# Performance work log

Hardware: AMD Instinct MI355X
Metric: run time of the kernel (lower is better)

Reference implementation:

```python
import jax, jax.numpy as jnp
import numpy as np
import math

D_MODEL = 2048
NUM_HEADS = 16
D_FF = 8192
HEAD_DIM = D_MODEL // NUM_HEADS
EPS = 1e-5


def _xavier(key, out_f, in_f):
    std = math.sqrt(2.0 / (in_f + out_f))
    return jax.random.normal(key, (out_f, in_f), dtype=jnp.float32) * std


def setup_inputs() -> dict:
    key = jax.random.key(0)
    ks = jax.random.split(key, 8)
    x = jax.random.normal(ks[0], (2, 2048, D_MODEL), dtype=jnp.float32)
    return {
        "x": x,
        "Wq": _xavier(ks[1], D_MODEL, D_MODEL),
        "Wk": _xavier(ks[2], D_MODEL, D_MODEL),
        "Wv": _xavier(ks[3], D_MODEL, D_MODEL),
        "Wo": _xavier(ks[4], D_MODEL, D_MODEL),
        "W1": _xavier(ks[5], D_FF, D_MODEL),
        "W2": _xavier(ks[6], D_MODEL, D_FF),
        "g1": jnp.ones((D_MODEL,), jnp.float32),
        "b1": jnp.zeros((D_MODEL,), jnp.float32),
        "g2": jnp.ones((D_MODEL,), jnp.float32),
        "b2": jnp.zeros((D_MODEL,), jnp.float32),
    }


def _ternary(w):
    # per-tensor abs-mean threshold -> {-1, 0, 1}
    abs_w = jnp.abs(w)
    thr = jnp.mean(abs_w)
    return jnp.where(abs_w > thr, jnp.sign(w), jnp.zeros_like(w))


def _tlin(x, w):
    # F.linear with ternarized weight [out, in], no bias
    return jnp.einsum("bsi,oi->bso", x, _ternary(w))


def _layernorm(x, g, b):
    mu = jnp.mean(x, axis=-1, keepdims=True)
    var = jnp.mean(jnp.square(x - mu), axis=-1, keepdims=True)
    return (x - mu) * jax.lax.rsqrt(var + EPS) * g + b


def reference(x, Wq, Wk, Wv, Wo, W1, W2, g1, b1, g2, b2):
    B, S, D = x.shape
    H, Hd = NUM_HEADS, HEAD_DIM
    q = _tlin(x, Wq).reshape(B, S, H, Hd).transpose(0, 2, 1, 3)  # bhsd
    k = _tlin(x, Wk).reshape(B, S, H, Hd).transpose(0, 2, 1, 3)
    v = _tlin(x, Wv).reshape(B, S, H, Hd).transpose(0, 2, 1, 3)
    scores = jnp.einsum("bhqd,bhkd->bhqk", q, k) / math.sqrt(Hd)
    probs = jax.nn.softmax(scores, axis=-1)
    attn = jnp.einsum("bhqk,bhkd->bhqd", probs, v)
    attn = attn.transpose(0, 2, 1, 3).reshape(B, S, D)
    attn = _tlin(attn, Wo)
    x = _layernorm(x + attn, g1, b1)  # dropout is identity in eval
    ff = _tlin(jax.nn.relu(_tlin(x, W1)), W2)
    x = _layernorm(x + ff, g2, b2)
    return x
```

## Files before the change

kernel.cpp:

```cpp
#include <hip/hip_runtime.h>
#include <hip/hip_bf16.h>

typedef __bf16 bf16_t;
typedef __bf16 bf16x8 __attribute__((ext_vector_type(8)));
typedef __bf16 bf16x4 __attribute__((ext_vector_type(4)));
typedef float f32x4 __attribute__((ext_vector_type(4)));
typedef int i32x4 __attribute__((ext_vector_type(4)));

__device__ __forceinline__ f32x4 mfma16(bf16x8 a, bf16x8 b, f32x4 c) {
  return __builtin_amdgcn_mfma_f32_16x16x32_bf16(a, b, c, 0, 0, 0);
}

__device__ __forceinline__ void gload16(const void* g, void* l) {
  __builtin_amdgcn_global_load_lds(
      (const __attribute__((address_space(1))) void*)g,
      (__attribute__((address_space(3))) void*)l, 16, 0, 0);
}

__global__ void abssum_all(const float* __restrict__ W0, const float* __restrict__ W1_,
                           const float* __restrict__ W2_, const float* __restrict__ W3,
                           const float* __restrict__ W4, const float* __restrict__ W5,
                           double* __restrict__ partial) {
  __shared__ double sd[256];
  const int w = blockIdx.y, tid = threadIdx.x;
  const float* W = (w == 0) ? W0 : (w == 1) ? W1_ : (w == 2) ? W2_ : (w == 3) ? W3 : (w == 4) ? W4 : W5;
  const int n4 = (w < 4) ? 1048576 : 4194304;
  double s = 0.0;
  for (int i = blockIdx.x * 256 + tid; i < n4; i += 262144) {
    float4 v = ((const float4*)W)[i];
    s += (double)fabsf(v.x); s += (double)fabsf(v.y);
    s += (double)fabsf(v.z); s += (double)fabsf(v.w);
  }
  sd[tid] = s; __syncthreads();
  for (int st = 128; st > 0; st >>= 1) { if (tid < st) sd[tid] += sd[tid + st]; __syncthreads(); }
  if (tid == 0) partial[w * 1024 + blockIdx.x] = sd[0];
}

__global__ void abssum_fin(const double* __restrict__ partial, double* __restrict__ sums) {
  __shared__ double sd[256];
  const int tid = threadIdx.x;
  const double* p = partial + blockIdx.x * 1024;
  double s = p[tid] + p[tid + 256] + p[tid + 512] + p[tid + 768];
  sd[tid] = s; __syncthreads();
  for (int st = 128; st > 0; st >>= 1) { if (tid < st) sd[tid] += sd[tid + st]; __syncthreads(); }
  if (tid == 0) sums[blockIdx.x] = sd[0];
}

__global__ void ternarize4(const float* __restrict__ W0, const float* __restrict__ W1_,
                           const float* __restrict__ W2_, const float* __restrict__ W3,
                           bf16_t* __restrict__ out, const double* __restrict__ sums) {
  const int w = blockIdx.x >> 12;
  const float* W = (w == 0) ? W0 : (w == 1) ? W1_ : (w == 2) ? W2_ : W3;
  const double thr = sums[w] / 4194304.0;
  const int i = (blockIdx.x & 4095) * 256 + threadIdx.x;
  float4 v = ((const float4*)W)[i];
  bf16x4 o;
  float t;
  t = ((double)fabsf(v.x) > thr) ? (v.x > 0.f ? 1.f : -1.f) : 0.f; o[0] = (bf16_t)t;
  t = ((double)fabsf(v.y) > thr) ? (v.y > 0.f ? 1.f : -1.f) : 0.f; o[1] = (bf16_t)t;
  t = ((double)fabsf(v.z) > thr) ? (v.z > 0.f ? 1.f : -1.f) : 0.f; o[2] = (bf16_t)t;
  t = ((double)fabsf(v.w) > thr) ? (v.w > 0.f ? 1.f : -1.f) : 0.f; o[3] = (bf16_t)t;
  *(bf16x4*)&out[(size_t)w * 4194304 + (size_t)i * 4] = o;
}

__global__ void ternarize_k(const float* __restrict__ W, bf16_t* __restrict__ out,
                            const double* __restrict__ sum, double n) {
  const double thr = sum[0] / n;
  const int i = blockIdx.x * 256 + threadIdx.x;
  float4 v = ((const float4*)W)[i];
  bf16x4 o;
  float t;
  t = ((double)fabsf(v.x) > thr) ? (v.x > 0.f ? 1.f : -1.f) : 0.f; o[0] = (bf16_t)t;
  t = ((double)fabsf(v.y) > thr) ? (v.y > 0.f ? 1.f : -1.f) : 0.f; o[1] = (bf16_t)t;
  t = ((double)fabsf(v.z) > thr) ? (v.z > 0.f ? 1.f : -1.f) : 0.f; o[2] = (bf16_t)t;
  t = ((double)fabsf(v.w) > thr) ? (v.w > 0.f ? 1.f : -1.f) : 0.f; o[3] = (bf16_t)t;
  *(bf16x4*)&out[(size_t)i * 4] = o;
}

__global__ void split_x_k(const float* __restrict__ X, bf16_t* __restrict__ xhl) {
  const int i = blockIdx.x * 256 + threadIdx.x;
  const int t = i >> 9, col = (i & 511) * 4;
  float4 v = ((const float4*)X)[i];
  bf16x4 h, l;
  h[0] = (bf16_t)v.x; l[0] = (bf16_t)(v.x - (float)h[0]);
  h[1] = (bf16_t)v.y; l[1] = (bf16_t)(v.y - (float)h[1]);
  h[2] = (bf16_t)v.z; l[2] = (bf16_t)(v.z - (float)h[2]);
  h[3] = (bf16_t)v.w; l[3] = (bf16_t)(v.w - (float)h[3]);
  *(bf16x4*)&xhl[(size_t)t * 4096 + col] = h;
  *(bf16x4*)&xhl[(size_t)t * 4096 + 2048 + col] = l;
}

template <int EPI>
__global__ __launch_bounds__(512, 2) void gemmP(
    const bf16_t* __restrict__ Ah, const bf16_t* __restrict__ Bw,
    void* __restrict__ C0, int N, int K, int lda) {
  constexpr int BM = 128;
  __shared__ __align__(16) bf16_t sA[3][BM * 64];
  __shared__ __align__(16) bf16_t sB[3][256 * 64];

  const int tid = threadIdx.x;
  const int wid = tid >> 6, lane = tid & 63, lr = lane & 15, lg = lane >> 4;
  const int wr = wid >> 2, wc = wid & 3;
  const size_t Ks = (size_t)K;

  const int nwg = gridDim.x * gridDim.y;
  const int bid0 = blockIdx.y * gridDim.x + blockIdx.x;
  const int swz = (bid0 & 7) * (nwg >> 3) + (bid0 >> 3);
  const int bx = swz % gridDim.x, by = swz / gridDim.x;
  const size_t m0 = (size_t)by * BM, n0 = (size_t)bx * 256;
  const int nt = K / 64;

  f32x4 acc[4][4] = {};

  auto STAGEH = [&](int bi, int kt, int half) {
    const size_t ko = (size_t)kt * 64;
    if (half == 0) {
#pragma unroll
      for (int i = 0; i < 2; i++) {
        const int t = i * 512 + tid;
        const int r = t >> 3;
        const int su = (t & 7) ^ (r & 7);
        const int lo = (i * 512 + wid * 64) * 8;
        gload16(Ah + (m0 + r) * (size_t)lda + ko + su * 8, (void*)&sA[bi][lo]);
      }
      {
        const int r = tid >> 3;
        const int su = (tid & 7) ^ (r & 7);
        gload16(Bw + (n0 + r) * Ks + ko + su * 8, (void*)&sB[bi][(wid * 64) * 8]);
      }
    } else {
#pragma unroll
      for (int i = 1; i < 4; i++) {
        const int t = i * 512 + tid;
        const int r = t >> 3;
        const int su = (t & 7) ^ (r & 7);
        gload16(Bw + (n0 + r) * Ks + ko + su * 8, (void*)&sB[bi][(i * 512 + wid * 64) * 8]);
      }
    }
  };
  auto LDA = [&](const bf16_t* base, int m, int k) -> bf16x8 {
    const int row = wr * 64 + m * 16 + lr;
    const int u = (k * 4 + lg) ^ (lr & 7);
    return *(const bf16x8*)&base[row * 64 + u * 8];
  };
  auto LDB = [&](const bf16_t* base, int n, int k) -> bf16x8 {
    const int row = wc * 64 + n * 16 + lr;
    const int u = (k * 4 + lg) ^ (lr & 7);
    return *(const bf16x8*)&base[row * 64 + u * 8];
  };

  STAGEH(0, 0, 0); STAGEH(0, 0, 1);
  STAGEH(1, 1, 0); STAGEH(1, 1, 1);
  asm volatile("s_waitcnt vmcnt(6)" ::: "memory");
  __builtin_amdgcn_s_barrier();

  int bc = 0, bs = 2;
  for (int kt = 0; kt < nt; kt++) {
    const bool pf = (kt + 2 < nt);
    bf16x8 a[4][2], bfr[4][2];
#pragma unroll
    for (int m = 0; m < 4; m++)
#pragma unroll
      for (int k = 0; k < 2; k++) a[m][k] = LDA(&sA[bc][0], m, k);
#pragma unroll
    for (int n = 0; n < 2; n++)
#pragma unroll
      for (int k = 0; k < 2; k++) bfr[n][k] = LDB(&sB[bc][0], n, k);
    if (pf) STAGEH(bs, kt + 2, 0);
    __builtin_amdgcn_s_barrier();
    asm volatile("s_waitcnt lgkmcnt(0)" ::: "memory");
    __builtin_amdgcn_sched_barrier(0);
    __builtin_amdgcn_s_setprio(1);
#pragma unroll
    for (int k = 0; k < 2; k++)
#pragma unroll
      for (int m = 0; m < 4; m++)
#pragma unroll
        for (int n = 0; n < 2; n++) acc[m][n] = mfma16(a[m][k], bfr[n][k], acc[m][n]);
    __builtin_amdgcn_s_setprio(0);
    __builtin_amdgcn_s_barrier();
#pragma unroll
    for (int n = 0; n < 2; n++)
#pragma unroll
      for (int k = 0; k < 2; k++) bfr[n + 2][k] = LDB(&sB[bc][0], n + 2, k);
    if (pf) STAGEH(bs, kt + 2, 1);
    if (kt + 1 < nt) {
      if (pf) asm volatile("s_waitcnt vmcnt(6)" ::: "memory");
      else    asm volatile("s_waitcnt vmcnt(0)" ::: "memory");
    }
    __builtin_amdgcn_s_barrier();
    asm volatile("s_waitcnt lgkmcnt(0)" ::: "memory");
    __builtin_amdgcn_sched_barrier(0);
    __builtin_amdgcn_s_setprio(1);
#pragma unroll
    for (int k = 0; k < 2; k++)
#pragma unroll
      for (int m = 0; m < 4; m++)
#pragma unroll
        for (int n = 0; n < 2; n++) acc[m][n + 2] = mfma16(a[m][k], bfr[n + 2][k], acc[m][n + 2]);
    __builtin_amdgcn_s_setprio(0);
    __builtin_amdgcn_s_barrier();
    bc = (bc + 1 == 3) ? 0 : bc + 1;
    bs = (bs + 1 == 3) ? 0 : bs + 1;
  }

  const int row0 = (int)m0 + wr * 64, colb = (int)n0 + wc * 64;
#pragma unroll
  for (int m = 0; m < 4; m++)
#pragma unroll
    for (int n = 0; n < 4; n++)
#pragma unroll
      for (int j = 0; j < 4; j++) {
        const int r = row0 + m * 16 + lg * 4 + j;
        const int c = colb + n * 16 + lr;
        const float v = acc[m][n][j];
        if constexpr (EPI == 1) {
          const int bb = r >> 11, ss = r & 2047;
          ((bf16_t*)C0)[((size_t)bb * 2048 + c) * 2048 + ss] = (bf16_t)v;
        } else {
          ((float*)C0)[(size_t)r * N + c] = v;
        }
      }
}

template <int EPI, int MB>
__global__ __launch_bounds__(512, 2) void gemm256(
    const bf16_t* __restrict__ A, const bf16_t* __restrict__ Bw,
    void* __restrict__ C0, void* __restrict__ C1,
    int N, int K, int lda, int ldb) {
  __shared__ __align__(16) bf16_t sA[2][256 * 64];
  __shared__ __align__(16) bf16_t sB[2][256 * 64];
  const int tid = threadIdx.x;
  const int wid = tid >> 6, lane = tid & 63, lr = lane & 15, lg = lane >> 4;
  const int wr = wid >> 2, wc = wid & 3;
  const int nwg = gridDim.x * gridDim.y;
  const int bid0 = blockIdx.y * gridDim.x + blockIdx.x;
  const int swz = (bid0 & 7) * (nwg >> 3) + (bid0 >> 3);
  const int bx = swz % gridDim.x, by = swz / gridDim.x;
  const int mt = by & ((1 << MB) - 1), kh = by >> MB;
  const int koff = kh * K;
  const size_t m0 = (size_t)mt * 256, n0 = (size_t)bx * 256;
  const int nt = K / 64;
  const bf16_t* Abase = A + m0 * (size_t)lda;
  const bf16_t* Bbase = Bw + n0 * (size_t)ldb;

  f32x4 acc[8][4] = {};

  auto SG = [&](const bf16_t* base, bf16_t* dst, int kt, int h, int ld) {
    const size_t co = (size_t)((kt * 64 + koff) & (ld - 1));
#pragma unroll
    for (int i = 0; i < 2; i++) {
      const int e = (2 * h + i) * 512 + tid;
      const int r = e >> 3;
      const int su = (tid & 7) ^ (r & 7);
      gload16(base + (size_t)r * ld + co + su * 8,
              (void*)&dst[((2 * h + i) * 512 + wid * 64) * 8]);
    }
  };
  auto LDA = [&](int bi, int m, int k) -> bf16x8 {
    const int row = wr * 128 + m * 16 + lr;
    const int u = (k * 4 + lg) ^ (lr & 7);
    return *(const bf16x8*)&sA[bi][row * 64 + u * 8];
  };
  auto LDB = [&](int bi, int n, int k) -> bf16x8 {
    const int row = wc * 64 + n * 16 + lr;
    const int u = (k * 4 + lg) ^ (lr & 7);
    return *(const bf16x8*)&sB[bi][row * 64 + u * 8];
  };

  SG(Abase, sA[0], 0, 0, lda); SG(Abase, sA[0], 0, 1, lda);
  SG(Bbase, sB[0], 0, 0, ldb); SG(Bbase, sB[0], 0, 1, ldb);
  SG(Bbase, sB[1], 1, 0, ldb); SG(Bbase, sB[1], 1, 1, ldb); SG(Abase, sA[1], 1, 0, lda);
  asm volatile("s_waitcnt vmcnt(6)" ::: "memory");
  __builtin_amdgcn_s_barrier();

  for (int kt = 0; kt < nt; kt++) {
    const int bi = kt & 1, bn = bi ^ 1;
    bf16x8 a[4][2], b[4][2];
#pragma unroll
    for (int m = 0; m < 4; m++)
#pragma unroll
      for (int k = 0; k < 2; k++) a[m][k] = LDA(bi, m, k);
#pragma unroll
    for (int n = 0; n < 2; n++)
#pragma unroll
      for (int k = 0; k < 2; k++) b[n][k] = LDB(bi, n, k);
    if (kt + 1 < nt) SG(Abase, sA[bn], kt + 1, 1, lda);
    __builtin_amdgcn_s_barrier();
    asm volatile("s_waitcnt lgkmcnt(0)" ::: "memory");
    __builtin_amdgcn_sched_barrier(0);
    __builtin_amdgcn_s_setprio(1);
#pragma unroll
    for (int k = 0; k < 2; k++)
#pragma unroll
      for (int m = 0; m < 4; m++)
#pragma unroll
        for (int n = 0; n < 2; n++) acc[m][n] = mfma16(a[m][k], b[n][k], acc[m][n]);
    __builtin_amdgcn_s_setprio(0);
    __builtin_amdgcn_s_barrier();
#pragma unroll
    for (int n = 0; n < 2; n++)
#pragma unroll
      for (int k = 0; k < 2; k++) b[n + 2][k] = LDB(bi, n + 2, k);
    if (kt + 2 < nt) SG(Bbase, sB[bi], kt + 2, 0, ldb);
    __builtin_amdgcn_s_barrier();
    asm volatile("s_waitcnt lgkmcnt(0)" ::: "memory");
    __builtin_amdgcn_sched_barrier(0);
    __builtin_amdgcn_s_setprio(1);
#pragma unroll
    for (int k = 0; k < 2; k++)
#pragma unroll
      for (int m = 0; m < 4; m++)
#pragma unroll
        for (int n = 0; n < 2; n++) acc[m][n + 2] = mfma16(a[m][k], b[n + 2][k], acc[m][n + 2]);
    __builtin_amdgcn_s_setprio(0);
    __builtin_amdgcn_s_barrier();
#pragma unroll
    for (int m = 0; m < 4; m++)
#pragma unroll
      for (int k = 0; k < 2; k++) a[m][k] = LDA(bi, m + 4, k);
    if (kt + 2 < nt) SG(Bbase, sB[bi], kt + 2, 1, ldb);
    __builtin_amdgcn_s_barrier();
    asm volatile("s_waitcnt lgkmcnt(0)" ::: "memory");
    __builtin_amdgcn_sched_barrier(0);
    __builtin_amdgcn_s_setprio(1);
#pragma unroll
    for (int k = 0; k < 2; k++)
#pragma unroll
      for (int m = 0; m < 4; m++)
#pragma unroll
        for (int n = 0; n < 2; n++) acc[m + 4][n + 2] = mfma16(a[m][k], b[n + 2][k], acc[m + 4][n + 2]);
    __builtin_amdgcn_s_setprio(0);
    __builtin_amdgcn_s_barrier();
    if (kt + 2 < nt) SG(Abase, sA[bi], kt + 2, 0, lda);
    __builtin_amdgcn_s_setprio(1);
#pragma unroll
    for (int k = 0; k < 2; k++)
#pragma unroll
      for (int m = 0; m < 4; m++)
#pragma unroll
        for (int n = 0; n < 2; n++) acc[m + 4][n] = mfma16(a[m][k], b[n][k], acc[m + 4][n]);
    __builtin_amdgcn_s_setprio(0);
    if (kt + 1 < nt) {
      if (kt + 2 < nt) asm volatile("s_waitcnt vmcnt(6)" ::: "memory");
      else             asm volatile("s_waitcnt vmcnt(0)" ::: "memory");
    }
    __builtin_amdgcn_s_barrier();
  }

  const int row0 = (int)m0 + wr * 128, colb = (int)n0 + wc * 64;
#pragma unroll
  for (int m = 0; m < 8; m++)
#pragma unroll
    for (int n = 0; n < 4; n++)
#pragma unroll
      for (int j = 0; j < 4; j++) {
        const int r = row0 + m * 16 + lg * 4 + j;
        const int c = colb + n * 16 + lr;
        const float v = acc[m][n][j];
        if constexpr (EPI == 0) {
          bf16_t hi = (bf16_t)v;
          ((bf16_t*)C0)[(size_t)r * N + c] = hi;
          ((bf16_t*)C1)[(size_t)r * N + c] = (bf16_t)(v - (float)hi);
        } else if constexpr (EPI == 4) {
          float* dst = (float*)(kh ? C1 : C0);
          dst[(size_t)r * N + c] = v;
        } else {
          ((bf16_t*)C0)[(size_t)r * N + c] = (bf16_t)fmaxf(v, 0.f);
        }
      }
}

__global__ __launch_bounds__(256, 2) void attn_k(
    const bf16_t* __restrict__ qh, const bf16_t* __restrict__ ql,
    const bf16_t* __restrict__ kh, const bf16_t* __restrict__ kl,
    const bf16_t* __restrict__ vT, bf16_t* __restrict__ out) {
  __shared__ __align__(16) bf16_t sKh[2 * 8192];
  __shared__ __align__(16) bf16_t sKl[2 * 8192];
  __shared__ __align__(16) bf16_t plds[4][2048];

  const int fid = blockIdx.y * 16 + blockIdx.x;
  const int qt = fid >> 5;
  const int bh = (fid & 7) * 4 + ((fid >> 3) & 3);
  const int b = bh >> 4, h = bh & 15;
  const int wv = threadIdx.x >> 6, lane = threadIdx.x & 63, lr = lane & 15, lg = lane >> 4;
  const size_t tok0 = (size_t)b * 2048 + qt * 128 + wv * 16;
  bf16_t* pw = &plds[wv][0];

  auto STAGE = [&](int bufi, int kv0n) {
#pragma unroll
    for (int i = 0; i < 4; i++) {
      const int tt = wv * 4 + i;
      const int r = tt * 4 + (lane >> 4);
      const int ce = ((lane & 15) ^ (r & 7)) * 8;
      const size_t gofs = ((size_t)b * 2048 + kv0n + r) * 4096 + h * 128 + ce;
      gload16(kh + gofs, (void*)&sKh[bufi * 8192 + tt * 512]);
      gload16(kl + gofs, (void*)&sKl[bufi * 8192 + tt * 512]);
    }
  };

  bf16x8 qhf[2][4], qlf[2][4];
#pragma unroll
  for (int t = 0; t < 2; t++) {
    const bf16_t* qp = qh + (tok0 + t * 64 + lr) * 4096 + h * 128 + lg * 8;
    const bf16_t* qp2 = ql + (tok0 + t * 64 + lr) * 4096 + h * 128 + lg * 8;
#pragma unroll
    for (int ks = 0; ks < 4; ks++) {
      qhf[t][ks] = *(const bf16x8*)(qp + ks * 32);
      qlf[t][ks] = *(const bf16x8*)(qp2 + ks * 32);
    }
  }
  f32x4 oacc[2][8] = {};
  float mrun[2] = {-1e30f, -1e30f};
  float lrun[2] = {0.f, 0.f};
  const bf16_t* vbase = vT + ((size_t)b * 2048 + h * 128) * 2048;
  const float sc = 0.08838834764831845f;
  const int swz8 = 2 * (lr & 7);

  STAGE(0, 0);
  for (int c = 0; c < 32; c++) {
    const int kv0 = c * 64;
    if (c + 1 < 32) {
      STAGE((c + 1) & 1, kv0 + 64);
      asm volatile("s_waitcnt vmcnt(8)" ::: "memory");
    } else {
      asm volatile("s_waitcnt vmcnt(0)" ::: "memory");
    }
    __builtin_amdgcn_s_barrier();

    const int bufo = (c & 1) * 8192;
    f32x4 s[2][4] = {};
    __builtin_amdgcn_s_setprio(1);
#pragma unroll
    for (int nb = 0; nb < 4; nb++) {
      const int rbase = bufo + (nb * 16 + lr) * 128;
#pragma unroll
      for (int ks = 0; ks < 4; ks++) {
        const int u = (((ks * 4 + lg) ^ (lr & 7)) * 8);
        bf16x8 kf = *(const bf16x8*)&sKh[rbase + u];
        bf16x8 kg = *(const bf16x8*)&sKl[rbase + u];
        s[0][nb] = mfma16(kf, qhf[0][ks], s[0][nb]);
        s[1][nb] = mfma16(kf, qhf[1][ks], s[1][nb]);
        s[0][nb] = mfma16(kf, qlf[0][ks], s[0][nb]);
        s[1][nb] = mfma16(kf, qlf[1][ks], s[1][nb]);
        s[0][nb] = mfma16(kg, qhf[0][ks], s[0][nb]);
        s[1][nb] = mfma16(kg, qhf[1][ks], s[1][nb]);
      }
    }
    __builtin_amdgcn_s_setprio(0);

    float resc[2];
    bool skip[2];
#pragma unroll
    for (int t = 0; t < 2; t++) {
#pragma unroll
      for (int nb = 0; nb < 4; nb++) s[t][nb] *= sc;
      f32x4 m4 = __builtin_elementwise_max(
          __builtin_elementwise_max(s[t][0], s[t][1]),
          __builtin_elementwise_max(s[t][2], s[t][3]));
      float mx = fmaxf(fmaxf(m4[0], m4[1]), fmaxf(m4[2], m4[3]));
      mx = fmaxf(mx, __shfl_xor(mx, 16));
      mx = fmaxf(mx, __shfl_xor(mx, 32));
      skip[t] = (__all(mx <= mrun[t] + 8.f) != 0);
      float rs_ = 1.f;
      if (!skip[t]) {
        const float mnew = fmaxf(mrun[t], mx);
        rs_ = __expf(mrun[t] - mnew);
        mrun[t] = mnew;
      }
      resc[t] = rs_;
      float ls = 0.f;
#pragma unroll
      for (int nb = 0; nb < 4; nb++) {
        bf16x4 pk;
#pragma unroll
        for (int j = 0; j < 4; j++) {
          const float p = __expf(s[t][nb][j] - mrun[t]);
          ls += p;
          pk[j] = (bf16_t)p;
        }
        const int s8 = (4 * nb + lg) ^ swz8;
        *(bf16x4*)&pw[t * 1024 + lr * 64 + s8 * 4] = pk;
      }
      ls += __shfl_xor(ls, 16);
      ls += __shfl_xor(ls, 32);
      lrun[t] = lrun[t] * rs_ + ls;
    }
    asm volatile("s_waitcnt lgkmcnt(0)" ::: "memory");
    __builtin_amdgcn_sched_barrier(0);
    bf16x8 pfr[2][2];
#pragma unroll
    for (int t = 0; t < 2; t++)
#pragma unroll
      for (int kc = 0; kc < 2; kc++) {
        const int se = (8 * kc + 2 * lg) ^ swz8;
        pfr[t][kc] = *(const bf16x8*)&pw[t * 1024 + lr * 64 + se * 4];
      }
    if (!skip[0]) {
#pragma unroll
      for (int dt = 0; dt < 8; dt++) oacc[0][dt] *= resc[0];
    }
    if (!skip[1]) {
#pragma unroll
      for (int dt = 0; dt < 8; dt++) oacc[1][dt] *= resc[1];
    }

    const bf16_t* vp = vbase + kv0 + lg * 8;
    __builtin_amdgcn_s_setprio(1);
#pragma unroll
    for (int dt = 0; dt < 8; dt++) {
      const bf16_t* vr = vp + (size_t)(dt * 16 + lr) * 2048;
      bf16x8 v0 = *(const bf16x8*)(vr);
      bf16x8 v1 = *(const bf16x8*)(vr + 32);
      oacc[0][dt] = mfma16(v0, pfr[0][0], oacc[0][dt]);
      oacc[1][dt] = mfma16(v0, pfr[1][0], oacc[1][dt]);
      oacc[0][dt] = mfma16(v1, pfr[0][1], oacc[0][dt]);
      oacc[1][dt] = mfma16(v1, pfr[1][1], oacc[1][dt]);
    }
    __builtin_amdgcn_s_setprio(0);
    asm volatile("" ::: "memory");
    __builtin_amdgcn_s_barrier();
  }

  {
    bf16_t* ep = &sKh[wv * 2176];
    const int q = lane >> 2, c4 = lane & 3;
    const int qs = 2 * (q & 7);
#pragma unroll
    for (int t = 0; t < 2; t++) {
      const float inv = 1.f / lrun[t];
#pragma unroll
      for (int dt = 0; dt < 8; dt++) {
        bf16x4 pk;
#pragma unroll
        for (int j = 0; j < 4; j++) pk[j] = (bf16_t)(oacc[t][dt][j] * inv);
        const int s5 = (4 * dt + lg) ^ swz8;
        *(bf16x4*)&ep[lr * 136 + s5 * 4] = pk;
      }
      asm volatile("s_waitcnt lgkmcnt(0)" ::: "memory");
      __builtin_amdgcn_sched_barrier(0);
      bf16_t* orow = out + (tok0 + t * 64 + q) * 2048 + h * 128 + c4 * 32;
#pragma unroll
      for (int i = 0; i < 4; i++) {
        const int se = (c4 * 8 + 2 * i) ^ qs;
        bf16x8 vv = *(const bf16x8*)&ep[q * 136 + se * 4];
        *(bf16x8*)(orow + i * 8) = vv;
      }
      asm volatile("s_waitcnt lgkmcnt(0)" ::: "memory");
    }
  }
}

__global__ __launch_bounds__(256) void ln_k(
    const float* __restrict__ X, const float* __restrict__ R,
    const float* __restrict__ G, const float* __restrict__ Bt,
    float* __restrict__ O32, bf16_t* __restrict__ O16) {
  const int t = blockIdx.x, tid = threadIdx.x;
  const float4* xp = (const float4*)(X + (size_t)t * 2048);
  const float4* rp = (const float4*)(R + (size_t)t * 2048);
  float4 v0 = xp[tid], w0 = rp[tid];
  float4 v1 = xp[tid + 256], w1 = rp[tid + 256];
  v0.x += w0.x; v0.y += w0.y; v0.z += w0.z; v0.w += w0.w;
  v1.x += w1.x; v1.y += w1.y; v1.z += w1.z; v1.w += w1.w;
  float sum = v0.x + v0.y + v0.z + v0.w + v1.x + v1.y + v1.z + v1.w;
  float sq = v0.x * v0.x + v0.y * v0.y + v0.z * v0.z + v0.w * v0.w +
             v1.x * v1.x + v1.y * v1.y + v1.z * v1.z + v1.w * v1.w;
  for (int d = 1; d < 64; d <<= 1) { sum += __shfl_xor(sum, d); sq += __shfl_xor(sq, d); }
  __shared__ float s1[4], s2[4];
  const int wv = tid >> 6, lane = tid & 63;
  if (lane == 0) { s1[wv] = sum; s2[wv] = sq; }
  __syncthreads();
  const float tot = s1[0] + s1[1] + s1[2] + s1[3];
  const float tsq = s2[0] + s2[1] + s2[2] + s2[3];
  const float mu = tot * (1.f / 2048.f);
  const float var = tsq * (1.f / 2048.f) - mu * mu;
  const float rs = 1.f / sqrtf(var + 1e-5f);
  const float4* gp = (const float4*)G;
  const float4* bp = (const float4*)Bt;
  float4 g0 = gp[tid], g1v = gp[tid + 256], b0 = bp[tid], b1v = bp[tid + 256];
  float4 o0, o1;
  o0.x = (v0.x - mu) * rs * g0.x + b0.x; o0.y = (v0.y - mu) * rs * g0.y + b0.y;
  o0.z = (v0.z - mu) * rs * g0.z + b0.z; o0.w = (v0.w - mu) * rs * g0.w + b0.w;
  o1.x = (v1.x - mu) * rs * g1v.x + b1v.x; o1.y = (v1.y - mu) * rs * g1v.y + b1v.y;
  o1.z = (v1.z - mu) * rs * g1v.z + b1v.z; o1.w = (v1.w - mu) * rs * g1v.w + b1v.w;
  if (O32) {
    ((float4*)(O32 + (size_t)t * 2048))[tid] = o0;
    ((float4*)(O32 + (size_t)t * 2048))[tid + 256] = o1;
  }
  if (O16) {
    bf16x4 h0, h1;
    h0[0] = (bf16_t)o0.x; h0[1] = (bf16_t)o0.y; h0[2] = (bf16_t)o0.z; h0[3] = (bf16_t)o0.w;
    h1[0] = (bf16_t)o1.x; h1[1] = (bf16_t)o1.y; h1[2] = (bf16_t)o1.z; h1[3] = (bf16_t)o1.w;
    *(bf16x4*)&O16[(size_t)t * 2048 + tid * 4] = h0;
    *(bf16x4*)&O16[(size_t)t * 2048 + 1024 + tid * 4] = h1;
  }
}

__global__ __launch_bounds__(256) void ln2_k(
    const bf16_t* __restrict__ Xb, const float* __restrict__ R0, const float* __restrict__ R1,
    const float* __restrict__ G, const float* __restrict__ Bt, float* __restrict__ out) {
  const int t = blockIdx.x, tid = threadIdx.x;
  bf16x4 x0 = *(const bf16x4*)&Xb[(size_t)t * 2048 + tid * 4];
  bf16x4 x1 = *(const bf16x4*)&Xb[(size_t)t * 2048 + 1024 + tid * 4];
  const float4* r0p = (const float4*)(R0 + (size_t)t * 2048);
  const float4* r1p = (const float4*)(R1 + (size_t)t * 2048);
  float4 a0 = r0p[tid], a1 = r0p[tid + 256];
  float4 c0 = r1p[tid], c1 = r1p[tid + 256];
  float4 v0, v1;
  v0.x = (float)x0[0] + a0.x + c0.x; v0.y = (float)x0[1] + a0.y + c0.y;
  v0.z = (float)x0[2] + a0.z + c0.z; v0.w = (float)x0[3] + a0.w + c0.w;
  v1.x = (float)x1[0] + a1.x + c1.x; v1.y = (float)x1[1] + a1.y + c1.y;
  v1.z = (float)x1[2] + a1.z + c1.z; v1.w = (float)x1[3] + a1.w + c1.w;
  float sum = v0.x + v0.y + v0.z + v0.w + v1.x + v1.y + v1.z + v1.w;
  float sq = v0.x * v0.x + v0.y * v0.y + v0.z * v0.z + v0.w * v0.w +
             v1.x * v1.x + v1.y * v1.y + v1.z * v1.z + v1.w * v1.w;
  for (int d = 1; d < 64; d <<= 1) { sum += __shfl_xor(sum, d); sq += __shfl_xor(sq, d); }
  __shared__ float s1[4], s2[4];
  const int wv = tid >> 6, lane = tid & 63;
  if (lane == 0) { s1[wv] = sum; s2[wv] = sq; }
  __syncthreads();
  const float tot = s1[0] + s1[1] + s1[2] + s1[3];
  const float tsq = s2[0] + s2[1] + s2[2] + s2[3];
  const float mu = tot * (1.f / 2048.f);
  const float var = tsq * (1.f / 2048.f) - mu * mu;
  const float rs = 1.f / sqrtf(var + 1e-5f);
  const float4* gp = (const float4*)G;
  const float4* bp = (const float4*)Bt;
  float4 g0 = gp[tid], g1v = gp[tid + 256], b0 = bp[tid], b1v = bp[tid + 256];
  float4 o0, o1;
  o0.x = (v0.x - mu) * rs * g0.x + b0.x; o0.y = (v0.y - mu) * rs * g0.y + b0.y;
  o0.z = (v0.z - mu) * rs * g0.z + b0.z; o0.w = (v0.w - mu) * rs * g0.w + b0.w;
  o1.x = (v1.x - mu) * rs * g1v.x + b1v.x; o1.y = (v1.y - mu) * rs * g1v.y + b1v.y;
  o1.z = (v1.z - mu) * rs * g1v.z + b1v.z; o1.w = (v1.w - mu) * rs * g1v.w + b1v.w;
  ((float4*)(out + (size_t)t * 2048))[tid] = o0;
  ((float4*)(out + (size_t)t * 2048))[tid + 256] = o1;
}

extern "C" void kernel_launch(void* const* d_in, const int* in_sizes, int n_in,
                              void* d_out, int out_size, void* d_ws, size_t ws_size,
                              hipStream_t stream) {
  const float* x  = (const float*)d_in[0];
  const float* Wq = (const float*)d_in[1];
  const float* Wk = (const float*)d_in[2];
  const float* Wv = (const float*)d_in[3];
  const float* Wo = (const float*)d_in[4];
  const float* W1 = (const float*)d_in[5];
  const float* W2 = (const float*)d_in[6];
  const float* g1 = (const float*)d_in[7];
  const float* b1 = (const float*)d_in[8];
  const float* g2 = (const float*)d_in[9];
  const float* b2 = (const float*)d_in[10];
  float* out = (float*)d_out;
  char* ws = (char*)d_ws;

  constexpr size_t SZB = (size_t)4096 * 2048 * 2;
  bf16_t* xhl = (bf16_t*)(ws + 0 * SZB);
  bf16_t* qkh = (bf16_t*)(ws + 2 * SZB);
  bf16_t* qkl = (bf16_t*)(ws + 4 * SZB);
  bf16_t* vt  = (bf16_t*)(ws + 6 * SZB);
  bf16_t* at  = (bf16_t*)(ws + 7 * SZB);
  float* o32  = (float*)(ws + 8 * SZB);
  bf16_t* wt  = (bf16_t*)(ws + 8 * SZB + (size_t)4096 * 2048 * 4);
  double* red = (double*)(ws + 8 * SZB + (size_t)4096 * 2048 * 4 + (size_t)8192 * 2048 * 2);
  double* sums = red + 8192;
  bf16_t* h1b = qkh;
  bf16_t* f1 = (bf16_t*)(ws + 4 * SZB);
  float* g32a = o32;
  float* g32b = (float*)(ws + 0 * SZB);
  (void)in_sizes; (void)n_in; (void)out_size; (void)ws_size;

  abssum_all<<<dim3(1024, 6), 256, 0, stream>>>(Wq, Wk, Wv, Wo, W1, W2, red);
  abssum_fin<<<6, 256, 0, stream>>>(red, sums);
  split_x_k<<<8192, 256, 0, stream>>>(x, xhl);
  ternarize4<<<16384, 256, 0, stream>>>(Wq, Wk, Wv, Wo, wt, sums);

  gemm256<0, 8><<<dim3(16, 16), 512, 0, stream>>>(xhl, wt, qkh, qkl, 4096, 4096, 4096, 2048);
  gemmP<1><<<dim3(8, 32), 512, 0, stream>>>(xhl, wt + 8388608, vt, 2048, 2048, 4096);
  attn_k<<<dim3(16, 32), 256, 0, stream>>>(qkh, qkl, qkh + 2048, qkl + 2048, vt, at);
  gemmP<2><<<dim3(8, 32), 512, 0, stream>>>(at, wt + 12582912, o32, 2048, 2048, 2048);
  ln_k<<<4096, 256, 0, stream>>>(x, o32, g1, b1, nullptr, h1b);
  ternarize_k<<<16384, 256, 0, stream>>>(W1, wt, sums + 4, 16777216.0);
  gemm256<3, 8><<<dim3(32, 16), 512, 0, stream>>>(h1b, wt, f1, nullptr, 8192, 2048, 2048, 2048);
  ternarize_k<<<16384, 256, 0, stream>>>(W2, wt, sums + 5, 16777216.0);
  gemm256<4, 4><<<dim3(8, 32), 512, 0, stream>>>(f1, wt, g32a, g32b, 2048, 4096, 8192, 8192);
  ln2_k<<<4096, 256, 0, stream>>>(h1b, g32a, g32b, g2, b2, out);
}
```

Measured before the change: 780.3 us.

## Fuse QKV projections into one GEMM and split-K the output projection

The Q/K and V projections now run as one wide GEMM launch. Its epilogue writes hi/lo bf16 split outputs for Q and K and a transposed bf16 V. The Wo projection moves from the 128-row gemmP kernel to the split-K gemm256 kernel, writing two fp32 partials that the new ln1 kernel sums along with the residual. This cuts launches, fills the GPU better with larger tiles, and removes the gemmP kernel. The cost is an extra fp32 partial buffer read in layernorm and a branchy epilogue.

After: 887.6 us. 1.14x slower.

```diff
diff --git a/kernel.cpp b/kernel.cpp
--- a/kernel.cpp
+++ b/kernel.cpp
@@ -90,143 +90,10 @@
   *(bf16x4*)&xhl[(size_t)t * 4096 + 2048 + col] = l;
 }
 
-template <int EPI>
-__global__ __launch_bounds__(512, 2) void gemmP(
-    const bf16_t* __restrict__ Ah, const bf16_t* __restrict__ Bw,
-    void* __restrict__ C0, int N, int K, int lda) {
-  constexpr int BM = 128;
-  __shared__ __align__(16) bf16_t sA[3][BM * 64];
-  __shared__ __align__(16) bf16_t sB[3][256 * 64];
-
-  const int tid = threadIdx.x;
-  const int wid = tid >> 6, lane = tid & 63, lr = lane & 15, lg = lane >> 4;
-  const int wr = wid >> 2, wc = wid & 3;
-  const size_t Ks = (size_t)K;
-
-  const int nwg = gridDim.x * gridDim.y;
-  const int bid0 = blockIdx.y * gridDim.x + blockIdx.x;
-  const int swz = (bid0 & 7) * (nwg >> 3) + (bid0 >> 3);
-  const int bx = swz % gridDim.x, by = swz / gridDim.x;
-  const size_t m0 = (size_t)by * BM, n0 = (size_t)bx * 256;
-  const int nt = K / 64;
-
-  f32x4 acc[4][4] = {};
-
-  auto STAGEH = [&](int bi, int kt, int half) {
-    const size_t ko = (size_t)kt * 64;
-    if (half == 0) {
-#pragma unroll
-      for (int i = 0; i < 2; i++) {
-        const int t = i * 512 + tid;
-        const int r = t >> 3;
-        const int su = (t & 7) ^ (r & 7);
-        const int lo = (i * 512 + wid * 64) * 8;
-        gload16(Ah + (m0 + r) * (size_t)lda + ko + su * 8, (void*)&sA[bi][lo]);
-      }
-      {
-        const int r = tid >> 3;
-        const int su = (tid & 7) ^ (r & 7);
-        gload16(Bw + (n0 + r) * Ks + ko + su * 8, (void*)&sB[bi][(wid * 64) * 8]);
-      }
-    } else {
-#pragma unroll
-      for (int i = 1; i < 4; i++) {
-        const int t = i * 512 + tid;
-        const int r = t >> 3;
-        const int su = (t & 7) ^ (r & 7);
-        gload16(Bw + (n0 + r) * Ks + ko + su * 8, (void*)&sB[bi][(i * 512 + wid * 64) * 8]);
-      }
-    }
-  };
-  auto LDA = [&](const bf16_t* base, int m, int k) -> bf16x8 {
-    const int row = wr * 64 + m * 16 + lr;
-    const int u = (k * 4 + lg) ^ (lr & 7);
-    return *(const bf16x8*)&base[row * 64 + u * 8];
-  };
-  auto LDB = [&](const bf16_t* base, int n, int k) -> bf16x8 {
-    const int row = wc * 64 + n * 16 + lr;
-    const int u = (k * 4 + lg) ^ (lr & 7);
-    return *(const bf16x8*)&base[row * 64 + u * 8];
-  };
-
-  STAGEH(0, 0, 0); STAGEH(0, 0, 1);
-  STAGEH(1, 1, 0); STAGEH(1, 1, 1);
-  asm volatile("s_waitcnt vmcnt(6)" ::: "memory");
-  __builtin_amdgcn_s_barrier();
-
-  int bc = 0, bs = 2;
-  for (int kt = 0; kt < nt; kt++) {
-    const bool pf = (kt + 2 < nt);
-    bf16x8 a[4][2], bfr[4][2];
-#pragma unroll
-    for (int m = 0; m < 4; m++)
-#pragma unroll
-      for (int k = 0; k < 2; k++) a[m][k] = LDA(&sA[bc][0], m, k);
-#pragma unroll
-    for (int n = 0; n < 2; n++)
-#pragma unroll
-      for (int k = 0; k < 2; k++) bfr[n][k] = LDB(&sB[bc][0], n, k);
-    if (pf) STAGEH(bs, kt + 2, 0);
-    __builtin_amdgcn_s_barrier();
-    asm volatile("s_waitcnt lgkmcnt(0)" ::: "memory");
-    __builtin_amdgcn_sched_barrier(0);
-    __builtin_amdgcn_s_setprio(1);
-#pragma unroll
-    for (int k = 0; k < 2; k++)
-#pragma unroll
-      for (int m = 0; m < 4; m++)
-#pragma unroll
-        for (int n = 0; n < 2; n++) acc[m][n] = mfma16(a[m][k], bfr[n][k], acc[m][n]);
-    __builtin_amdgcn_s_setprio(0);
-    __builtin_amdgcn_s_barrier();
-#pragma unroll
-    for (int n = 0; n < 2; n++)
-#pragma unroll
-      for (int k = 0; k < 2; k++) bfr[n + 2][k] = LDB(&sB[bc][0], n + 2, k);
-    if (pf) STAGEH(bs, kt + 2, 1);
-    if (kt + 1 < nt) {
-      if (pf) asm volatile("s_waitcnt vmcnt(6)" ::: "memory");
-      else    asm volatile("s_waitcnt vmcnt(0)" ::: "memory");
-    }
-    __builtin_amdgcn_s_barrier();
-    asm volatile("s_waitcnt lgkmcnt(0)" ::: "memory");
-    __builtin_amdgcn_sched_barrier(0);
-    __builtin_amdgcn_s_setprio(1);
-#pragma unroll
-    for (int k = 0; k < 2; k++)
-#pragma unroll
-      for (int m = 0; m < 4; m++)
-#pragma unroll
-        for (int n = 0; n < 2; n++) acc[m][n + 2] = mfma16(a[m][k], bfr[n + 2][k], acc[m][n + 2]);
-    __builtin_amdgcn_s_setprio(0);
-    __builtin_amdgcn_s_barrier();
-    bc = (bc + 1 == 3) ? 0 : bc + 1;
-    bs = (bs + 1 == 3) ? 0 : bs + 1;
-  }
-
-  const int row0 = (int)m0 + wr * 64, colb = (int)n0 + wc * 64;
-#pragma unroll
-  for (int m = 0; m < 4; m++)
-#pragma unroll
-    for (int n = 0; n < 4; n++)
-#pragma unroll
-      for (int j = 0; j < 4; j++) {
-        const int r = row0 + m * 16 + lg * 4 + j;
-        const int c = colb + n * 16 + lr;
-        const float v = acc[m][n][j];
-        if constexpr (EPI == 1) {
-          const int bb = r >> 11, ss = r & 2047;
-          ((bf16_t*)C0)[((size_t)bb * 2048 + c) * 2048 + ss] = (bf16_t)v;
-        } else {
-          ((float*)C0)[(size_t)r * N + c] = v;
-        }
-      }
-}
-
 template <int EPI, int MB>
 __global__ __launch_bounds__(512, 2) void gemm256(
     const bf16_t* __restrict__ A, const bf16_t* __restrict__ Bw,
-    void* __restrict__ C0, void* __restrict__ C1,
+    void* __restrict__ C0, void* __restrict__ C1, void* __restrict__ C2,
     int N, int K, int lda, int ldb) {
   __shared__ __align__(16) bf16_t sA[2][256 * 64];
   __shared__ __align__(16) bf16_t sB[2][256 * 64];
@@ -358,10 +225,15 @@
         const int r = row0 + m * 16 + lg * 4 + j;
         const int c = colb + n * 16 + lr;
         const float v = acc[m][n][j];
-        if constexpr (EPI == 0) {
-          bf16_t hi = (bf16_t)v;
-          ((bf16_t*)C0)[(size_t)r * N + c] = hi;
-          ((bf16_t*)C1)[(size_t)r * N + c] = (bf16_t)(v - (float)hi);
+        if constexpr (EPI == 5) {
+          if (c < 4096) {
+            bf16_t hi = (bf16_t)v;
+            ((bf16_t*)C0)[(size_t)r * 4096 + c] = hi;
+            ((bf16_t*)C1)[(size_t)r * 4096 + c] = (bf16_t)(v - (float)hi);
+          } else {
+            const int bb = r >> 11, ss = r & 2047;
+            ((bf16_t*)C2)[((size_t)bb * 2048 + (c - 4096)) * 2048 + ss] = (bf16_t)v;
+          }
         } else if constexpr (EPI == 4) {
           float* dst = (float*)(kh ? C1 : C0);
           dst[(size_t)r * N + c] = v;
@@ -551,17 +423,18 @@
   }
 }
 
-__global__ __launch_bounds__(256) void ln_k(
-    const float* __restrict__ X, const float* __restrict__ R,
-    const float* __restrict__ G, const float* __restrict__ Bt,
-    float* __restrict__ O32, bf16_t* __restrict__ O16) {
+__global__ __launch_bounds__(256) void ln1_k(
+    const float* __restrict__ X, const float* __restrict__ R0, const float* __restrict__ R1,
+    const float* __restrict__ G, const float* __restrict__ Bt, bf16_t* __restrict__ O16) {
   const int t = blockIdx.x, tid = threadIdx.x;
   const float4* xp = (const float4*)(X + (size_t)t * 2048);
-  const float4* rp = (const float4*)(R + (size_t)t * 2048);
-  float4 v0 = xp[tid], w0 = rp[tid];
-  float4 v1 = xp[tid + 256], w1 = rp[tid + 256];
-  v0.x += w0.x; v0.y += w0.y; v0.z += w0.z; v0.w += w0.w;
-  v1.x += w1.x; v1.y += w1.y; v1.z += w1.z; v1.w += w1.w;
+  const float4* r0p = (const float4*)(R0 + (size_t)t * 2048);
+  const float4* r1p = (const float4*)(R1 + (size_t)t * 2048);
+  float4 v0 = xp[tid], v1 = xp[tid + 256];
+  float4 a0 = r0p[tid], a1 = r0p[tid + 256];
+  float4 c0 = r1p[tid], c1 = r1p[tid + 256];
+  v0.x += a0.x + c0.x; v0.y += a0.y + c0.y; v0.z += a0.z + c0.z; v0.w += a0.w + c0.w;
+  v1.x += a1.x + c1.x; v1.y += a1.y + c1.y; v1.z += a1.z + c1.z; v1.w += a1.w + c1.w;
   float sum = v0.x + v0.y + v0.z + v0.w + v1.x + v1.y + v1.z + v1.w;
   float sq = v0.x * v0.x + v0.y * v0.y + v0.z * v0.z + v0.w * v0.w +
              v1.x * v1.x + v1.y * v1.y + v1.z * v1.z + v1.w * v1.w;
@@ -578,22 +451,17 @@
   const float4* gp = (const float4*)G;
   const float4* bp = (const float4*)Bt;
   float4 g0 = gp[tid], g1v = gp[tid + 256], b0 = bp[tid], b1v = bp[tid + 256];
-  float4 o0, o1;
-  o0.x = (v0.x - mu) * rs * g0.x + b0.x; o0.y = (v0.y - mu) * rs * g0.y + b0.y;
-  o0.z = (v0.z - mu) * rs * g0.z + b0.z; o0.w = (v0.w - mu) * rs * g0.w + b0.w;
-  o1.x = (v1.x - mu) * rs * g1v.x + b1v.x; o1.y = (v1.y - mu) * rs * g1v.y + b1v.y;
-  o1.z = (v1.z - mu) * rs * g1v.z + b1v.z; o1.w = (v1.w - mu) * rs * g1v.w + b1v.w;
-  if (O32) {
-    ((float4*)(O32 + (size_t)t * 2048))[tid] = o0;
-    ((float4*)(O32 + (size_t)t * 2048))[tid + 256] = o1;
-  }
-  if (O16) {
-    bf16x4 h0, h1;
-    h0[0] = (bf16_t)o0.x; h0[1] = (bf16_t)o0.y; h0[2] = (bf16_t)o0.z; h0[3] = (bf16_t)o0.w;
-    h1[0] = (bf16_t)o1.x; h1[1] = (bf16_t)o1.y; h1[2] = (bf16_t)o1.z; h1[3] = (bf16_t)o1.w;
-    *(bf16x4*)&O16[(size_t)t * 2048 + tid * 4] = h0;
-    *(bf16x4*)&O16[(size_t)t * 2048 + 1024 + tid * 4] = h1;
-  }
+  bf16x4 h0, h1;
+  h0[0] = (bf16_t)((v0.x - mu) * rs * g0.x + b0.x);
+  h0[1] = (bf16_t)((v0.y - mu) * rs * g0.y + b0.y);
+  h0[2] = (bf16_t)((v0.z - mu) * rs * g0.z + b0.z);
+  h0[3] = (bf16_t)((v0.w - mu) * rs * g0.w + b0.w);
+  h1[0] = (bf16_t)((v1.x - mu) * rs * g1v.x + b1v.x);
+  h1[1] = (bf16_t)((v1.y - mu) * rs * g1v.y + b1v.y);
+  h1[2] = (bf16_t)((v1.z - mu) * rs * g1v.z + b1v.z);
+  h1[3] = (bf16_t)((v1.w - mu) * rs * g1v.w + b1v.w);
+  *(bf16x4*)&O16[(size_t)t * 2048 + tid * 4] = h0;
+  *(bf16x4*)&O16[(size_t)t * 2048 + 1024 + tid * 4] = h1;
 }
 
 __global__ __launch_bounds__(256) void ln2_k(
@@ -665,8 +533,8 @@
   double* sums = red + 8192;
   bf16_t* h1b = qkh;
   bf16_t* f1 = (bf16_t*)(ws + 4 * SZB);
-  float* g32a = o32;
-  float* g32b = (float*)(ws + 0 * SZB);
+  float* p0 = o32;
+  float* p1 = (float*)(ws + 0 * SZB);
   (void)in_sizes; (void)n_in; (void)out_size; (void)ws_size;
 
   abssum_all<<<dim3(1024, 6), 256, 0, stream>>>(Wq, Wk, Wv, Wo, W1, W2, red);
@@ -674,14 +542,13 @@
   split_x_k<<<8192, 256, 0, stream>>>(x, xhl);
   ternarize4<<<16384, 256, 0, stream>>>(Wq, Wk, Wv, Wo, wt, sums);
 
-  gemm256<0, 8><<<dim3(16, 16), 512, 0, stream>>>(xhl, wt, qkh, qkl, 4096, 4096, 4096, 2048);
-  gemmP<1><<<dim3(8, 32), 512, 0, stream>>>(xhl, wt + 8388608, vt, 2048, 2048, 4096);
+  gemm256<5, 8><<<dim3(24, 16), 512, 0, stream>>>(xhl, wt, qkh, qkl, vt, 6144, 4096, 4096, 2048);
   attn_k<<<dim3(16, 32), 256, 0, stream>>>(qkh, qkl, qkh + 2048, qkl + 2048, vt, at);
-  gemmP<2><<<dim3(8, 32), 512, 0, stream>>>(at, wt + 12582912, o32, 2048, 2048, 2048);
-  ln_k<<<4096, 256, 0, stream>>>(x, o32, g1, b1, nullptr, h1b);
+  gemm256<4, 4><<<dim3(8, 32), 512, 0, stream>>>(at, wt + 12582912, p0, p1, nullptr, 2048, 1024, 2048, 2048);
+  ln1_k<<<4096, 256, 0, stream>>>(x, p0, p1, g1, b1, h1b);
   ternarize_k<<<16384, 256, 0, stream>>>(W1, wt, sums + 4, 16777216.0);
-  gemm256<3, 8><<<dim3(32, 16), 512, 0, stream>>>(h1b, wt, f1, nullptr, 8192, 2048, 2048, 2048);
+  gemm256<3, 8><<<dim3(32, 16), 512, 0, stream>>>(h1b, wt, f1, nullptr, nullptr, 8192, 2048, 2048, 2048);
   ternarize_k<<<16384, 256, 0, stream>>>(W2, wt, sums + 5, 16777216.0);
-  gemm256<4, 4><<<dim3(8, 32), 512, 0, stream>>>(f1, wt, g32a, g32b, 2048, 4096, 8192, 8192);
-  ln2_k<<<4096, 256, 0, stream>>>(h1b, g32a, g32b, g2, b2, out);
-}
+  gemm256<4, 4><<<dim3(8, 32), 512, 0, stream>>>(f1, wt, p0, p1, nullptr, 2048, 4096, 8192, 8192);
+  ln2_k<<<4096, 256, 0, stream>>>(h1b, p0, p1, g2, b2, out);
+}
```
